# Optimization experiments

Hardware: AMD Instinct MI355X
Metric: run time of the kernel (lower is better)

The kernel has to match this reference:

```python
import jax, jax.numpy as jnp
import numpy as np

B, DIM, H, W = 16, 256, 64, 64
HEADS, DHEAD, MEM = 4, 32, 4
HIDDEN = HEADS * DHEAD


def setup_inputs() -> dict:
    key = jax.random.key(0)
    ks = jax.random.split(key, 4)
    return {
        "x": jax.random.normal(ks[0], (B, DIM, H, W), dtype=jnp.float32),
        "g1": jnp.ones((DIM,), dtype=jnp.float32),
        "w_qkv": jax.random.normal(ks[1], (3 * HIDDEN, DIM), dtype=jnp.float32) * 0.02,
        "mem_kv": jax.random.normal(ks[2], (2, HEADS, DHEAD, MEM), dtype=jnp.float32),
        "w_out": jax.random.normal(ks[3], (DIM, HIDDEN), dtype=jnp.float32) * 0.02,
        "b_out": jnp.zeros((DIM,), dtype=jnp.float32),
        "g2": jnp.ones((DIM,), dtype=jnp.float32),
    }


def _rmsnorm(x, g):
    # F.normalize(x, dim=1) * g * sqrt(dim); g broadcast over (1, dim, 1, 1)
    n = jnp.sqrt(jnp.sum(x * x, axis=1, keepdims=True))
    scale = jnp.asarray(x.shape[1], x.dtype) ** 0.5
    return x / jnp.maximum(n, 1e-12) * g[None, :, None, None] * scale


def reference(x, g1, w_qkv, mem_kv, w_out, b_out, g2):
    b, c, h, w = x.shape
    attn_scale = DHEAD ** -0.5
    xn = _rmsnorm(x, g1)
    # 1x1 conv == channel matmul; chunk(3, dim=1) -> leading axis 3 after reshape
    qkv = jnp.einsum('oc,bchw->bohw', w_qkv, xn)
    qkv = qkv.reshape(b, 3, HEADS, DHEAD, h * w)  # b 3 h d n
    q, k, v = qkv[:, 0], qkv[:, 1], qkv[:, 2]
    mk = jnp.broadcast_to(mem_kv[0][None], (b, HEADS, DHEAD, MEM))
    mv = jnp.broadcast_to(mem_kv[1][None], (b, HEADS, DHEAD, MEM))
    k = jnp.concatenate([mk, k], axis=-1)  # b h d (m+n)
    v = jnp.concatenate([mv, v], axis=-1)
    q = jax.nn.softmax(q, axis=-2) * attn_scale  # softmax over feature dim d
    k = jax.nn.softmax(k, axis=-1)               # softmax over token dim n
    context = jnp.einsum('bhdn,bhen->bhde', k, v)  # d x e per head
    out = jnp.einsum('bhde,bhdn->bhen', context, q)
    out = out.reshape(b, HIDDEN, h, w)
    out = jnp.einsum('oc,bchw->bohw', w_out, out) + b_out[None, :, None, None]
    return _rmsnorm(out, g2)
```

## Files before the change

kernel.cpp:

```cpp
#include <hip/hip_runtime.h>
#include <hip/hip_bf16.h>

#define NB 16
#define DIM 256
#define HW 4096
#define HEADS 4
#define DHEAD 32
#define MEM 4
#define HIDDEN 128

typedef __hip_bfloat16 bf16;
typedef __attribute__((ext_vector_type(8))) short bf16x8;
typedef __attribute__((ext_vector_type(4))) float f32x4;
typedef __attribute__((ext_vector_type(4))) unsigned short us4;

#define AS1 __attribute__((address_space(1)))
#define AS3 __attribute__((address_space(3)))

__device__ __forceinline__ void gld_lds16(const void* g, void* l) {
    __builtin_amdgcn_global_load_lds((const AS1 void*)g, (AS3 void*)l, 16, 0, 0);
}
__device__ __forceinline__ float b2f(short s) {
    union { unsigned int u; float f; } x; x.u = ((unsigned int)(unsigned short)s) << 16; return x.f;
}
__device__ __forceinline__ short f2bs(float f) {
    bf16 h = __float2bfloat16(f);
    return *reinterpret_cast<short*>(&h);
}

constexpr size_t OFF_W1B  = 0;
constexpr size_t OFF_R    = OFF_W1B + 98304*2;
constexpr size_t OFF_RP   = OFF_R + 65536*4;
constexpr size_t OFF_PCTX = OFF_RP + 4*65536*4;
constexpr size_t OFF_CTXN = OFF_PCTX + (size_t)32*64*1056*4;
constexpr size_t OFF_M    = OFF_CTXN + (size_t)64*1024*4;
constexpr size_t OFF_QT   = OFF_M + (size_t)NB*DIM*HIDDEN*2;
constexpr size_t OFF_XT   = OFF_QT + (size_t)NB*HW*HIDDEN*2;

__global__ void k_prep(const float* __restrict__ wqkv, const float* __restrict__ g1,
                       short* __restrict__ w1b) {
    int i = blockIdx.x * 256 + threadIdx.x;
    w1b[i] = f2bs(wqkv[i] * g1[i & (DIM - 1)]);
}

__global__ __launch_bounds__(256) void k_tr(const float* __restrict__ x,
                                            short* __restrict__ xT,
                                            float* __restrict__ rpart) {
    int n0 = blockIdx.x * 64, cy = blockIdx.y, b = blockIdx.z;
    int c0 = cy * 64;
    __shared__ short xs[64 * 65];
    __shared__ float ps[4][64];
    int t = threadIdx.x;
    int ln = t & 63, cb = t >> 6;
    const float* xp = x + ((size_t)b * DIM + c0) * HW + n0;
    float ss = 0.f;
#pragma unroll
    for (int j = 0; j < 16; ++j) {
        int c = cb * 16 + j;
        float v = xp[(size_t)c * HW + ln];
        ss += v * v;
        xs[c * 65 + ln] = f2bs(v);
    }
    ps[cb][ln] = ss;
    __syncthreads();
    if (t < 64)
        rpart[((size_t)cy * NB + b) * HW + n0 + t] = ps[0][t] + ps[1][t] + ps[2][t] + ps[3][t];
    int n = t >> 2, ch = t & 3;
    alignas(16) short tmp[16];
#pragma unroll
    for (int i = 0; i < 16; ++i) tmp[i] = xs[(ch * 16 + i) * 65 + n];
    short* o = xT + ((size_t)b * HW + n0 + n) * DIM + c0 + ch * 16;
    *(bf16x8*)(o)     = *(bf16x8*)(tmp);
    *(bf16x8*)(o + 8) = *(bf16x8*)(tmp + 8);
}

__global__ void k_rfin(const float* __restrict__ rpart, float* __restrict__ r) {
    int i = blockIdx.x * 256 + threadIdx.x;
    float s = rpart[i] + rpart[65536 + i] + rpart[131072 + i] + rpart[196608 + i];
    r[i] = 16.0f / fmaxf(sqrtf(s), 1e-12f);
}

__global__ __launch_bounds__(768) void k_gemm(const short* __restrict__ w1b,
                                              const short* __restrict__ xT,
                                              const float* __restrict__ r,
                                              short* __restrict__ qT,
                                              float* __restrict__ pctx) {
    __shared__ __align__(16) char smem[65536];
    int nt = blockIdx.x, b = blockIdx.y;
    int t = threadIdx.x;
    int w = t >> 6, lane = t & 63;
    int wr = w >> 1, wc = w & 1;
    int lr = lane & 15, lg = lane >> 4;
    const f32x4 fz = {0.f, 0.f, 0.f, 0.f};
    f32x4 acc[4][4];
#pragma unroll
    for (int m = 0; m < 4; ++m)
#pragma unroll
        for (int n = 0; n < 4; ++n) acc[m][n] = fz;

    const short* Bg = xT + ((size_t)b * HW + nt * 128) * 256;

    for (int kt = 0; kt < 4; ++kt) {
        int kk = kt * 64;
        if (kt) __syncthreads();
#pragma unroll
        for (int is = 0; is < 4; ++is) {
            int o = is * 12288 + t * 16;
            int row = o >> 7;
            int js = ((o >> 4) & 7) ^ (row & 7);
            gld_lds16(w1b + (size_t)row * 256 + kk + js * 8, smem + o);
        }
        {
            int o = t * 16;
            int row = o >> 7;
            int js = ((o >> 4) & 7) ^ (row & 7);
            gld_lds16(Bg + (size_t)row * 256 + kk + js * 8, smem + 49152 + o);
        }
        if (t < 256) {
            int o = 12288 + t * 16;
            int row = o >> 7;
            int js = ((o >> 4) & 7) ^ (row & 7);
            gld_lds16(Bg + (size_t)row * 256 + kk + js * 8, smem + 49152 + o);
        }
        __syncthreads();
#pragma unroll
        for (int ks = 0; ks < 2; ++ks) {
            int j = lg + 4 * ks;
            bf16x8 av[4], bv[4];
#pragma unroll
            for (int m = 0; m < 4; ++m) {
                int row = wr * 64 + m * 16 + lr;
                av[m] = *(const bf16x8*)(smem + row * 128 + ((j ^ (row & 7)) << 4));
            }
#pragma unroll
            for (int nf = 0; nf < 4; ++nf) {
                int row = wc * 64 + nf * 16 + lr;
                bv[nf] = *(const bf16x8*)(smem + 49152 + row * 128 + ((j ^ (row & 7)) << 4));
            }
#pragma unroll
            for (int m = 0; m < 4; ++m)
#pragma unroll
                for (int nf = 0; nf < 4; ++nf)
                    acc[m][nf] = __builtin_amdgcn_mfma_f32_16x16x32_bf16(av[m], bv[nf], acc[m][nf], 0, 0, 0);
        }
    }

    int gcol0 = nt * 128 + wc * 64 + lr;
    float rv[4];
#pragma unroll
    for (int nf = 0; nf < 4; ++nf) rv[nf] = r[(size_t)b * HW + gcol0 + nf * 16];

    __syncthreads();
    short* ekb = (short*)smem;
    short* vb  = (short*)(smem + 32768);

    if (wr < 2) {
#pragma unroll
        for (int nf = 0; nf < 4; ++nf) {
            int gcol = gcol0 + nf * 16;
#pragma unroll
            for (int a = 0; a < 2; ++a) {
                float v[8];
#pragma unroll
                for (int mm = 0; mm < 2; ++mm)
#pragma unroll
                    for (int q = 0; q < 4; ++q)
                        v[mm * 4 + q] = acc[2 * a + mm][nf][q] * rv[nf];
                float mx = v[0];
#pragma unroll
                for (int i = 1; i < 8; ++i) mx = fmaxf(mx, v[i]);
                mx = fmaxf(mx, __shfl_xor(mx, 16));
                mx = fmaxf(mx, __shfl_xor(mx, 32));
                float sum = 0.f;
#pragma unroll
                for (int i = 0; i < 8; ++i) { v[i] = __expf(v[i] - mx); sum += v[i]; }
                sum += __shfl_xor(sum, 16);
                sum += __shfl_xor(sum, 32);
                float inv = 0.17677669529663689f / sum;
                size_t base = ((size_t)b * HW + gcol) * 128 + (wr * 2 + a) * 32 + lg * 4;
#pragma unroll
                for (int mm = 0; mm < 2; ++mm) {
                    us4 pk;
#pragma unroll
                    for (int q = 0; q < 4; ++q)
                        pk[q] = (unsigned short)f2bs(v[mm * 4 + q] * inv);
                    *(us4*)(qT + base + mm * 16) = pk;
                }
            }
        }
    } else if (wr < 4) {
#pragma unroll
        for (int m = 0; m < 4; ++m)
#pragma unroll
            for (int nf = 0; nf < 4; ++nf)
#pragma unroll
                for (int q = 0; q < 4; ++q) {
                    int rloc = (wr - 2) * 64 + m * 16 + lg * 4 + q;
                    int col = wc * 64 + nf * 16 + lr;
                    int cs = ((((col >> 3) ^ (rloc & 15)) << 3) | (col & 7));
                    ekb[rloc * 128 + cs] = f2bs(__expf(acc[m][nf][q] * rv[nf]));
                }
    } else {
#pragma unroll
        for (int m = 0; m < 4; ++m)
#pragma unroll
            for (int nf = 0; nf < 4; ++nf)
#pragma unroll
                for (int q = 0; q < 4; ++q) {
                    int rloc = (wr - 4) * 64 + m * 16 + lg * 4 + q;
                    int col = wc * 64 + nf * 16 + lr;
                    int cs = ((((col >> 3) ^ (rloc & 15)) << 3) | (col & 7));
                    vb[rloc * 128 + cs] = f2bs(acc[m][nf][q] * rv[nf]);
                }
    }
    __syncthreads();
    if (w < 4) {
        int h = w;
        f32x4 c2[2][2];
        c2[0][0] = fz; c2[0][1] = fz; c2[1][0] = fz; c2[1][1] = fz;
#pragma unroll
        for (int ks = 0; ks < 4; ++ks) {
            int j = ks * 4 + lg;
            bf16x8 a2[2], b2[2];
#pragma unroll
            for (int mm = 0; mm < 2; ++mm) {
                int row = h * 32 + mm * 16 + lr;
                a2[mm] = *(const bf16x8*)(ekb + row * 128 + ((j ^ (row & 15)) << 3));
            }
#pragma unroll
            for (int nn = 0; nn < 2; ++nn) {
                int row = h * 32 + nn * 16 + lr;
                b2[nn] = *(const bf16x8*)(vb + row * 128 + ((j ^ (row & 15)) << 3));
            }
#pragma unroll
            for (int mm = 0; mm < 2; ++mm)
#pragma unroll
                for (int nn = 0; nn < 2; ++nn)
                    c2[mm][nn] = __builtin_amdgcn_mfma_f32_16x16x32_bf16(a2[mm], b2[nn], c2[mm][nn], 0, 0, 0);
        }
        float* o = pctx + ((size_t)nt * 64 + b * 4 + h) * 1056;
#pragma unroll
        for (int mm = 0; mm < 2; ++mm)
#pragma unroll
            for (int nn = 0; nn < 2; ++nn)
#pragma unroll
                for (int qq = 0; qq < 4; ++qq) {
                    int d = mm * 16 + lg * 4 + qq;
                    int e = nn * 16 + lr;
                    o[d * 32 + e] = c2[mm][nn][qq];
                }
    } else if (w >= 8) {
        int hd = (w - 8) * 32 + (lane & 31);
        int half = lane >> 5;
        float rs = 0.f;
#pragma unroll
        for (int blk = 0; blk < 8; ++blk) {
            int chunk = half * 8 + blk;
            bf16x8 e8 = *(const bf16x8*)(ekb + hd * 128 + ((chunk ^ (hd & 15)) << 3));
#pragma unroll
            for (int jj = 0; jj < 8; ++jj) rs += b2f(e8[jj]);
        }
        rs += __shfl_xor(rs, 32);
        if (lane < 32)
            pctx[((size_t)nt * 64 + b * 4 + (w - 8)) * 1056 + 1024 + (lane & 31)] = rs;
    }
}

__global__ __launch_bounds__(256) void k_red(const float* __restrict__ pctx,
                                             const float* __restrict__ memkv,
                                             float* __restrict__ ctxn) {
    int ds = blockIdx.x, bh = blockIdx.y;
    int t = threadIdx.x;
    int dd = t >> 5, ee = t & 31;
    int d = ds * 8 + dd;
    int h = bh & 3;
    __shared__ float rss[8];
    float s = 0.f;
#pragma unroll 8
    for (int c = 0; c < 32; ++c)
        s += pctx[((size_t)c * 64 + bh) * 1056 + d * 32 + ee];
    if (t < 8) {
        int d2 = ds * 8 + t;
        float rs = 0.f;
#pragma unroll 8
        for (int c = 0; c < 32; ++c)
            rs += pctx[((size_t)c * 64 + bh) * 1056 + 1024 + d2];
#pragma unroll
        for (int m2 = 0; m2 < MEM; ++m2) rs += __expf(memkv[(h * 32 + d2) * MEM + m2]);
        rss[t] = rs;
    }
    float mem = 0.f;
#pragma unroll
    for (int m2 = 0; m2 < MEM; ++m2)
        mem += __expf(memkv[(h * 32 + d) * MEM + m2]) * memkv[512 + (h * 32 + ee) * MEM + m2];
    __syncthreads();
    ctxn[(size_t)bh * 1024 + d * 32 + ee] = (s + mem) / rss[dd];
}

__global__ __launch_bounds__(256) void k_M2(const float* __restrict__ ctxn,
                                            const float* __restrict__ wout,
                                            short* __restrict__ Mmat) {
    int og = blockIdx.x, b = blockIdx.y;
    __shared__ float ctx[4 * 33 * 33];
    __shared__ float wsw[32 * 136];
    int t = threadIdx.x;
#pragma unroll
    for (int j = 0; j < 16; ++j) {
        int e = t + j * 256;
        int h = e >> 10, dd = (e >> 5) & 31, ee = e & 31;
        ctx[h * 1089 + dd * 33 + ee] = ctxn[(size_t)(b * 4 + h) * 1024 + (e & 1023)];
    }
#pragma unroll
    for (int j = 0; j < 4; ++j) {
        int e4 = t + j * 256;
        int row = e4 >> 5, c = (e4 & 31) * 4;
        f32x4 w4 = *(const f32x4*)(wout + (size_t)(og * 32 + row) * HIDDEN + c);
        *(f32x4*)(wsw + row * 136 + (c >> 5) * 34 + (c & 31)) = w4;
    }
    __syncthreads();
    int ol = t >> 3, hg = t & 7;
    alignas(16) short out16[16];
#pragma unroll
    for (int ii = 0; ii < 16; ++ii) {
        int hd = hg * 16 + ii;
        int h = hd >> 5, dd = hd & 31;
        float s = 0.f;
#pragma unroll
        for (int e = 0; e < 32; ++e)
            s += wsw[ol * 136 + h * 34 + e] * ctx[h * 1089 + dd * 33 + e];
        out16[ii] = f2bs(s);
    }
    short* op = Mmat + ((size_t)(b * 256 + og * 32 + ol)) * 128 + hg * 16;
    *(bf16x8*)(op)     = *(bf16x8*)(out16);
    *(bf16x8*)(op + 8) = *(bf16x8*)(out16 + 8);
}

__global__ __launch_bounds__(256) void k_out2(const short* __restrict__ Mmat,
                                              const short* __restrict__ qT,
                                              const float* __restrict__ bout,
                                              const float* __restrict__ g2,
                                              float* __restrict__ out) {
    int nt = blockIdx.x, b = blockIdx.y;
    __shared__ short As[256 * 64];
    __shared__ short Bs[64 * 64];
    __shared__ float sw[4][80];
    __shared__ float r2s[64];
    int t = threadIdx.x;
    int wave = t >> 6, lane = t & 63;
    int lr = lane & 15, lg = lane >> 4;
    const short* Ag = Mmat + (size_t)b * 256 * 128;
    const short* Bg = qT + ((size_t)b * HW + nt * 64) * 128;
    const f32x4 fz = {0.f, 0.f, 0.f, 0.f};
    f32x4 acc[4][4];
#pragma unroll
    for (int m = 0; m < 4; ++m)
#pragma unroll
        for (int n = 0; n < 4; ++n) acc[m][n] = fz;

    for (int kk = 0; kk < 128; kk += 64) {
        if (kk) __syncthreads();
#pragma unroll
        for (int is = 0; is < 8; ++is) {
            int o = is * 4096 + t * 16;
            int rr2 = o >> 7;
            int js = ((o >> 4) & 7) ^ (rr2 & 7);
            gld_lds16(Ag + (size_t)rr2 * 128 + kk + js * 8, (char*)As + o);
        }
#pragma unroll
        for (int is = 0; is < 2; ++is) {
            int o = is * 4096 + t * 16;
            int rr2 = o >> 7;
            int js = ((o >> 4) & 7) ^ (rr2 & 7);
            gld_lds16(Bg + (size_t)rr2 * 128 + kk + js * 8, (char*)Bs + o);
        }
        __syncthreads();
#pragma unroll
        for (int ks = 0; ks < 2; ++ks) {
            bf16x8 av[4], bv[4];
            int j = lg + 4 * ks;
#pragma unroll
            for (int m = 0; m < 4; ++m) {
                int row = wave * 64 + m * 16 + lr;
                av[m] = *(const bf16x8*)((const char*)As + row * 128 + ((j ^ (row & 7)) << 4));
            }
#pragma unroll
            for (int n = 0; n < 4; ++n) {
                int row = n * 16 + lr;
                bv[n] = *(const bf16x8*)((const char*)Bs + row * 128 + ((j ^ (row & 7)) << 4));
            }
#pragma unroll
            for (int m = 0; m < 4; ++m)
#pragma unroll
                for (int n = 0; n < 4; ++n)
                    acc[m][n] = __builtin_amdgcn_mfma_f32_16x16x32_bf16(av[m], bv[n], acc[m][n], 0, 0, 0);
        }
    }
    float bb[4][4], gg[4][4];
#pragma unroll
    for (int m = 0; m < 4; ++m)
#pragma unroll
        for (int q = 0; q < 4; ++q) {
            int row = wave * 64 + m * 16 + lg * 4 + q;
            bb[m][q] = bout[row];
            gg[m][q] = g2[row];
        }
    float ssn[4] = {0.f, 0.f, 0.f, 0.f};
#pragma unroll
    for (int n = 0; n < 4; ++n)
#pragma unroll
        for (int m = 0; m < 4; ++m)
#pragma unroll
            for (int q = 0; q < 4; ++q) {
                float val = acc[m][n][q] + bb[m][q];
                acc[m][n][q] = val;
                ssn[n] += val * val;
            }
#pragma unroll
    for (int n = 0; n < 4; ++n) {
        ssn[n] += __shfl_xor(ssn[n], 16);
        ssn[n] += __shfl_xor(ssn[n], 32);
    }
    if (lg == 0) {
#pragma unroll
        for (int n = 0; n < 4; ++n) sw[wave][n * 16 + lr] = ssn[n];
    }
    __syncthreads();
    if (t < 64) {
        float s = sw[0][t] + sw[1][t] + sw[2][t] + sw[3][t];
        r2s[t] = 16.0f / fmaxf(sqrtf(s), 1e-12f);
    }
    __syncthreads();
    float* op = out + (size_t)b * DIM * HW + nt * 64;
#pragma unroll
    for (int n = 0; n < 4; ++n) {
        float rc = r2s[n * 16 + lr];
#pragma unroll
        for (int m = 0; m < 4; ++m)
#pragma unroll
            for (int q = 0; q < 4; ++q) {
                int row = wave * 64 + m * 16 + lg * 4 + q;
                op[(size_t)row * HW + n * 16 + lr] = acc[m][n][q] * rc * gg[m][q];
            }
    }
}

extern "C" void kernel_launch(void* const* d_in, const int* in_sizes, int n_in,
                              void* d_out, int out_size, void* d_ws, size_t ws_size,
                              hipStream_t stream) {
    const float* x     = (const float*)d_in[0];
    const float* g1    = (const float*)d_in[1];
    const float* wqkv  = (const float*)d_in[2];
    const float* memkv = (const float*)d_in[3];
    const float* wout  = (const float*)d_in[4];
    const float* bout  = (const float*)d_in[5];
    const float* g2    = (const float*)d_in[6];
    float* out = (float*)d_out;
    char* ws = (char*)d_ws;

    short* w1b  = (short*)(ws + OFF_W1B);
    float* r    = (float*)(ws + OFF_R);
    float* rpart= (float*)(ws + OFF_RP);
    float* pctx = (float*)(ws + OFF_PCTX);
    float* ctxn = (float*)(ws + OFF_CTXN);
    short* Mmat = (short*)(ws + OFF_M);
    short* qT   = (short*)(ws + OFF_QT);
    short* xT   = (short*)(ws + OFF_XT);

    k_prep<<<384, 256, 0, stream>>>(wqkv, g1, w1b);
    k_tr<<<dim3(64, 4, NB), 256, 0, stream>>>(x, xT, rpart);
    k_rfin<<<256, 256, 0, stream>>>(rpart, r);
    k_gemm<<<dim3(32, NB), 768, 0, stream>>>(w1b, xT, r, qT, pctx);
    k_red<<<dim3(4, 64), 256, 0, stream>>>(pctx, memkv, ctxn);
    k_M2<<<dim3(8, NB), 256, 0, stream>>>(ctxn, wout, Mmat);
    k_out2<<<dim3(64, NB), 256, 0, stream>>>(Mmat, qT, bout, g2, out);
}
```

Baseline: 80.18 us.

## Fold rms finalize into QKV GEMM and load full-K B tile once

```diff
diff --git a/kernel.cpp b/kernel.cpp
--- a/kernel.cpp
+++ b/kernel.cpp
@@ -29,8 +29,7 @@
 }
 
 constexpr size_t OFF_W1B  = 0;
-constexpr size_t OFF_R    = OFF_W1B + 98304*2;
-constexpr size_t OFF_RP   = OFF_R + 65536*4;
+constexpr size_t OFF_RP   = OFF_W1B + 98304*2;
 constexpr size_t OFF_PCTX = OFF_RP + 4*65536*4;
 constexpr size_t OFF_CTXN = OFF_PCTX + (size_t)32*64*1056*4;
 constexpr size_t OFF_M    = OFF_CTXN + (size_t)64*1024*4;
@@ -74,18 +73,13 @@
     *(bf16x8*)(o + 8) = *(bf16x8*)(tmp + 8);
 }
 
-__global__ void k_rfin(const float* __restrict__ rpart, float* __restrict__ r) {
-    int i = blockIdx.x * 256 + threadIdx.x;
-    float s = rpart[i] + rpart[65536 + i] + rpart[131072 + i] + rpart[196608 + i];
-    r[i] = 16.0f / fmaxf(sqrtf(s), 1e-12f);
-}
-
 __global__ __launch_bounds__(768) void k_gemm(const short* __restrict__ w1b,
                                               const short* __restrict__ xT,
-                                              const float* __restrict__ r,
+                                              const float* __restrict__ rpart,
                                               short* __restrict__ qT,
                                               float* __restrict__ pctx) {
-    __shared__ __align__(16) char smem[65536];
+    __shared__ __align__(16) char smem[66048];
+    float* r2s = (float*)(smem + 65536);
     int nt = blockIdx.x, b = blockIdx.y;
     int t = threadIdx.x;
     int w = t >> 6, lane = t & 63;
@@ -98,57 +92,54 @@
 #pragma unroll
         for (int n = 0; n < 4; ++n) acc[m][n] = fz;
 
+    if (t < 128) {
+        int col = nt * 128 + t;
+        float s = rpart[(size_t)b * HW + col] + rpart[(size_t)(16 + b) * HW + col]
+                + rpart[(size_t)(32 + b) * HW + col] + rpart[(size_t)(48 + b) * HW + col];
+        r2s[t] = 16.0f / fmaxf(sqrtf(s), 1e-12f);
+    }
+
     const short* Bg = xT + ((size_t)b * HW + nt * 128) * 256;
-
-    for (int kt = 0; kt < 4; ++kt) {
-        int kk = kt * 64;
-        if (kt) __syncthreads();
-#pragma unroll
-        for (int is = 0; is < 4; ++is) {
-            int o = is * 12288 + t * 16;
-            int row = o >> 7;
-            int js = ((o >> 4) & 7) ^ (row & 7);
-            gld_lds16(w1b + (size_t)row * 256 + kk + js * 8, smem + o);
-        }
-        {
-            int o = t * 16;
-            int row = o >> 7;
-            int js = ((o >> 4) & 7) ^ (row & 7);
-            gld_lds16(Bg + (size_t)row * 256 + kk + js * 8, smem + 49152 + o);
-        }
-        if (t < 256) {
-            int o = 12288 + t * 16;
-            int row = o >> 7;
-            int js = ((o >> 4) & 7) ^ (row & 7);
-            gld_lds16(Bg + (size_t)row * 256 + kk + js * 8, smem + 49152 + o);
-        }
-        __syncthreads();
-#pragma unroll
-        for (int ks = 0; ks < 2; ++ks) {
-            int j = lg + 4 * ks;
-            bf16x8 av[4], bv[4];
-#pragma unroll
-            for (int m = 0; m < 4; ++m) {
-                int row = wr * 64 + m * 16 + lr;
-                av[m] = *(const bf16x8*)(smem + row * 128 + ((j ^ (row & 7)) << 4));
-            }
-#pragma unroll
-            for (int nf = 0; nf < 4; ++nf) {
-                int row = wc * 64 + nf * 16 + lr;
-                bv[nf] = *(const bf16x8*)(smem + 49152 + row * 128 + ((j ^ (row & 7)) << 4));
-            }
-#pragma unroll
-            for (int m = 0; m < 4; ++m)
-#pragma unroll
-                for (int nf = 0; nf < 4; ++nf)
-                    acc[m][nf] = __builtin_amdgcn_mfma_f32_16x16x32_bf16(av[m], bv[nf], acc[m][nf], 0, 0, 0);
-        }
+#pragma unroll
+    for (int is = 0; is < 5; ++is) {
+        int o = is * 12288 + t * 16;
+        int row = o >> 9;
+        int js = ((o >> 4) & 31) ^ (row & 31);
+        gld_lds16(Bg + (size_t)row * 256 + js * 8, smem + o);
+    }
+    if (t < 256) {
+        int o = 61440 + t * 16;
+        int row = o >> 9;
+        int js = ((o >> 4) & 31) ^ (row & 31);
+        gld_lds16(Bg + (size_t)row * 256 + js * 8, smem + o);
+    }
+    __syncthreads();
+
+    const short* Ag = w1b + (size_t)(wr * 64 + lr) * 256 + lg * 8;
+#pragma unroll 2
+    for (int kt = 0; kt < 8; ++kt) {
+        int kk = kt * 32;
+        bf16x8 av[4], bv[4];
+#pragma unroll
+        for (int m = 0; m < 4; ++m)
+            av[m] = *(const bf16x8*)(Ag + (size_t)m * 16 * 256 + kk);
+#pragma unroll
+        for (int nf = 0; nf < 4; ++nf) {
+            int row = wc * 64 + nf * 16 + lr;
+            int phys = (kt * 4 + lg) ^ (row & 31);
+            bv[nf] = *(const bf16x8*)(smem + row * 512 + phys * 16);
+        }
+#pragma unroll
+        for (int m = 0; m < 4; ++m)
+#pragma unroll
+            for (int nf = 0; nf < 4; ++nf)
+                acc[m][nf] = __builtin_amdgcn_mfma_f32_16x16x32_bf16(av[m], bv[nf], acc[m][nf], 0, 0, 0);
     }
 
     int gcol0 = nt * 128 + wc * 64 + lr;
     float rv[4];
 #pragma unroll
-    for (int nf = 0; nf < 4; ++nf) rv[nf] = r[(size_t)b * HW + gcol0 + nf * 16];
+    for (int nf = 0; nf < 4; ++nf) rv[nf] = r2s[wc * 64 + nf * 16 + lr];
 
     __syncthreads();
     short* ekb = (short*)smem;
@@ -458,7 +449,6 @@
     char* ws = (char*)d_ws;
 
     short* w1b  = (short*)(ws + OFF_W1B);
-    float* r    = (float*)(ws + OFF_R);
     float* rpart= (float*)(ws + OFF_RP);
     float* pctx = (float*)(ws + OFF_PCTX);
     float* ctxn = (float*)(ws + OFF_CTXN);
@@ -468,8 +458,7 @@
 
     k_prep<<<384, 256, 0, stream>>>(wqkv, g1, w1b);
     k_tr<<<dim3(64, 4, NB), 256, 0, stream>>>(x, xT, rpart);
-    k_rfin<<<256, 256, 0, stream>>>(rpart, r);
-    k_gemm<<<dim3(32, NB), 768, 0, stream>>>(w1b, xT, r, qT, pctx);
+    k_gemm<<<dim3(32, NB), 768, 0, stream>>>(w1b, xT, rpart, qT, pctx);
     k_red<<<dim3(4, 64), 256, 0, stream>>>(pctx, memkv, ctxn);
     k_M2<<<dim3(8, NB), 256, 0, stream>>>(ctxn, wout, Mmat);
     k_out2<<<dim3(64, NB), 256, 0, stream>>>(Mmat, qT, bout, g2, out);
```

Result: slower. 91.56 us (+14.2%).

## Double-buffer GEMM LDS staging and fold norm finalization into GEMM

Applied to the files above, without the earlier changes.

```diff
diff --git a/kernel.cpp b/kernel.cpp
--- a/kernel.cpp
+++ b/kernel.cpp
@@ -29,8 +29,7 @@
 }
 
 constexpr size_t OFF_W1B  = 0;
-constexpr size_t OFF_R    = OFF_W1B + 98304*2;
-constexpr size_t OFF_RP   = OFF_R + 65536*4;
+constexpr size_t OFF_RP   = OFF_W1B + 98304*2;
 constexpr size_t OFF_PCTX = OFF_RP + 4*65536*4;
 constexpr size_t OFF_CTXN = OFF_PCTX + (size_t)32*64*1056*4;
 constexpr size_t OFF_M    = OFF_CTXN + (size_t)64*1024*4;
@@ -74,18 +73,12 @@
     *(bf16x8*)(o + 8) = *(bf16x8*)(tmp + 8);
 }
 
-__global__ void k_rfin(const float* __restrict__ rpart, float* __restrict__ r) {
-    int i = blockIdx.x * 256 + threadIdx.x;
-    float s = rpart[i] + rpart[65536 + i] + rpart[131072 + i] + rpart[196608 + i];
-    r[i] = 16.0f / fmaxf(sqrtf(s), 1e-12f);
-}
-
-__global__ __launch_bounds__(768) void k_gemm(const short* __restrict__ w1b,
-                                              const short* __restrict__ xT,
-                                              const float* __restrict__ r,
-                                              short* __restrict__ qT,
-                                              float* __restrict__ pctx) {
-    __shared__ __align__(16) char smem[65536];
+__global__ __launch_bounds__(768, 1) void k_gemm(const short* __restrict__ w1b,
+                                                 const short* __restrict__ xT,
+                                                 const float* __restrict__ rpart,
+                                                 short* __restrict__ qT,
+                                                 float* __restrict__ pctx) {
+    extern __shared__ __align__(16) char smem[];
     int nt = blockIdx.x, b = blockIdx.y;
     int t = threadIdx.x;
     int w = t >> 6, lane = t & 63;
@@ -100,29 +93,42 @@
 
     const short* Bg = xT + ((size_t)b * HW + nt * 128) * 256;
 
-    for (int kt = 0; kt < 4; ++kt) {
+    auto STAGE = [&](int kt, int buf) {
         int kk = kt * 64;
-        if (kt) __syncthreads();
+        char* asb = smem + buf * 49152;
+        char* bsb = smem + 98304 + buf * 16384;
 #pragma unroll
         for (int is = 0; is < 4; ++is) {
             int o = is * 12288 + t * 16;
             int row = o >> 7;
             int js = ((o >> 4) & 7) ^ (row & 7);
-            gld_lds16(w1b + (size_t)row * 256 + kk + js * 8, smem + o);
+            gld_lds16(w1b + (size_t)row * 256 + kk + js * 8, asb + o);
         }
         {
             int o = t * 16;
             int row = o >> 7;
             int js = ((o >> 4) & 7) ^ (row & 7);
-            gld_lds16(Bg + (size_t)row * 256 + kk + js * 8, smem + 49152 + o);
+            gld_lds16(Bg + (size_t)row * 256 + kk + js * 8, bsb + o);
         }
         if (t < 256) {
             int o = 12288 + t * 16;
             int row = o >> 7;
             int js = ((o >> 4) & 7) ^ (row & 7);
-            gld_lds16(Bg + (size_t)row * 256 + kk + js * 8, smem + 49152 + o);
-        }
-        __syncthreads();
+            gld_lds16(Bg + (size_t)row * 256 + kk + js * 8, bsb + o);
+        }
+    };
+
+    STAGE(0, 0);
+    asm volatile("s_waitcnt vmcnt(0)" ::: "memory");
+    __builtin_amdgcn_s_barrier();
+
+#pragma unroll
+    for (int kt = 0; kt < 4; ++kt) {
+        int buf = kt & 1;
+        if (kt < 3) STAGE(kt + 1, buf ^ 1);
+        const char* asb = smem + buf * 49152;
+        const char* bsb = smem + 98304 + buf * 16384;
+        __builtin_amdgcn_s_setprio(1);
 #pragma unroll
         for (int ks = 0; ks < 2; ++ks) {
             int j = lg + 4 * ks;
@@ -130,12 +136,12 @@
 #pragma unroll
             for (int m = 0; m < 4; ++m) {
                 int row = wr * 64 + m * 16 + lr;
-                av[m] = *(const bf16x8*)(smem + row * 128 + ((j ^ (row & 7)) << 4));
+                av[m] = *(const bf16x8*)(asb + row * 128 + ((j ^ (row & 7)) << 4));
             }
 #pragma unroll
             for (int nf = 0; nf < 4; ++nf) {
                 int row = wc * 64 + nf * 16 + lr;
-                bv[nf] = *(const bf16x8*)(smem + 49152 + row * 128 + ((j ^ (row & 7)) << 4));
+                bv[nf] = *(const bf16x8*)(bsb + row * 128 + ((j ^ (row & 7)) << 4));
             }
 #pragma unroll
             for (int m = 0; m < 4; ++m)
@@ -143,14 +149,21 @@
                 for (int nf = 0; nf < 4; ++nf)
                     acc[m][nf] = __builtin_amdgcn_mfma_f32_16x16x32_bf16(av[m], bv[nf], acc[m][nf], 0, 0, 0);
         }
+        __builtin_amdgcn_s_setprio(0);
+        asm volatile("s_waitcnt vmcnt(0)" ::: "memory");
+        __builtin_amdgcn_s_barrier();
     }
 
     int gcol0 = nt * 128 + wc * 64 + lr;
     float rv[4];
 #pragma unroll
-    for (int nf = 0; nf < 4; ++nf) rv[nf] = r[(size_t)b * HW + gcol0 + nf * 16];
-
-    __syncthreads();
+    for (int nf = 0; nf < 4; ++nf) {
+        int col = gcol0 + nf * 16;
+        float s = rpart[(size_t)b * HW + col] + rpart[(size_t)(16 + b) * HW + col]
+                + rpart[(size_t)(32 + b) * HW + col] + rpart[(size_t)(48 + b) * HW + col];
+        rv[nf] = 16.0f / fmaxf(sqrtf(s), 1e-12f);
+    }
+
     short* ekb = (short*)smem;
     short* vb  = (short*)(smem + 32768);
 
@@ -458,7 +471,6 @@
     char* ws = (char*)d_ws;
 
     short* w1b  = (short*)(ws + OFF_W1B);
-    float* r    = (float*)(ws + OFF_R);
     float* rpart= (float*)(ws + OFF_RP);
     float* pctx = (float*)(ws + OFF_PCTX);
     float* ctxn = (float*)(ws + OFF_CTXN);
@@ -466,10 +478,12 @@
     short* qT   = (short*)(ws + OFF_QT);
     short* xT   = (short*)(ws + OFF_XT);
 
+    hipFuncSetAttribute((const void*)k_gemm,
+                        hipFuncAttributeMaxDynamicSharedMemorySize, 131072);
+
     k_prep<<<384, 256, 0, stream>>>(wqkv, g1, w1b);
     k_tr<<<dim3(64, 4, NB), 256, 0, stream>>>(x, xT, rpart);
-    k_rfin<<<256, 256, 0, stream>>>(rpart, r);
-    k_gemm<<<dim3(32, NB), 768, 0, stream>>>(w1b, xT, r, qT, pctx);
+    k_gemm<<<dim3(32, NB), 768, 131072, stream>>>(w1b, xT, rpart, qT, pctx);
     k_red<<<dim3(4, 64), 256, 0, stream>>>(pctx, memkv, ctxn);
     k_M2<<<dim3(8, NB), 256, 0, stream>>>(ctxn, wout, Mmat);
     k_out2<<<dim3(64, NB), 256, 0, stream>>>(Mmat, qT, bout, g2, out);
```

After: 78.09 us. 2.6% less time.
